# Kernel tuning notes

Hardware: AMD Instinct MI355X
Metric: run time of the kernel (lower is better)

The kernel has to match this reference:

```python
import jax, jax.numpy as jnp
import numpy as np

B, S, C, H = 64, 512, 256, 128
P = S  # predict_length defaults to seq_length


def _linear_init(k, fan_in, fan_out):
    bound = 1.0 / np.sqrt(fan_in)
    kw, kb = jax.random.split(k)
    w = jax.random.uniform(kw, (fan_in, fan_out), minval=-bound, maxval=bound, dtype=jnp.float32)
    b = jax.random.uniform(kb, (fan_out,), minval=-bound, maxval=bound, dtype=jnp.float32)
    return w, b


def setup_inputs() -> dict:
    key = jax.random.key(0)
    ks = jax.random.split(key, 10)
    x = jax.random.normal(ks[0], (B, S, C), dtype=jnp.float32)
    wq1, bq1 = _linear_init(ks[1], S, H)
    wk1, bk1 = _linear_init(ks[2], S, H)
    wq2, bq2 = _linear_init(ks[3], S // 2, H)
    wk2, bk2 = _linear_init(ks[4], S // 2, H)
    wq3, bq3 = _linear_init(ks[5], S // 4, H)
    wk3, bk3 = _linear_init(ks[6], S // 4, H)
    wv, bv = _linear_init(ks[7], S, S)
    wo, bo = _linear_init(ks[8], S, P)
    return dict(x=x, wq1=wq1, bq1=bq1, wk1=wk1, bk1=bk1,
                wq2=wq2, bq2=bq2, wk2=wk2, bk2=bk2,
                wq3=wq3, bq3=bq3, wk3=wk3, bk3=bk3,
                wv=wv, bv=bv, wo=wo, bo=bo)


def _channel_attn(xl, wq, bq, wk, bk):
    # xl: [b', C, L]; q,k: [b', C, H]; returns softmax channel-attention [b', C, C]
    q = xl @ wq + bq
    k = xl @ wk + bk
    scores = jnp.einsum('bch,bdh->bcd', q, k) / jnp.sqrt(jnp.asarray(H, q.dtype))
    return jax.nn.softmax(scores, axis=-1)


def reference(x, wq1, bq1, wk1, bk1, wq2, bq2, wk2, bk2, wq3, bq3, wk3, bk3, wv, bv, wo, bo):
    b, s, c = x.shape
    x1 = jnp.swapaxes(x, -2, -1)                                   # [B, C, S]
    x2 = jnp.swapaxes(x.reshape(b * 2, s // 2, c), -2, -1)          # [2B, C, S/2]
    x3 = jnp.swapaxes(x.reshape(b * 4, s // 4, c), -2, -1)          # [4B, C, S/4]
    a1 = _channel_attn(x1, wq1, bq1, wk1, bk1)                      # [B, C, C]
    a2 = _channel_attn(x2, wq2, bq2, wk2, bk2).reshape(b, 2, c, c).mean(axis=1)
    a3 = _channel_attn(x3, wq3, bq3, wk3, bk3).reshape(b, 4, c, c).mean(axis=1)
    stacked = jnp.stack([a1, a2, a3], axis=0)                       # [3, B, C, C]
    gate = jax.nn.softmax(stacked, axis=0)                          # softmax over scales
    attn = (stacked * gate).sum(axis=0)                             # gated multi-scale combine [B, C, C]
    v = x1 @ wv + bv                                                # [B, C, S]
    out = (attn @ v) @ wo + bo                                      # [B, C, P]
    return jnp.swapaxes(out, -2, -1)                                # [B, P, C]
```

## Files before the change

kernel.cpp:

```cpp
#include <hip/hip_runtime.h>
#include <hip/hip_bf16.h>


typedef __attribute__((ext_vector_type(8))) short bf16x8;
typedef __attribute__((ext_vector_type(4))) float f32x4;
typedef __attribute__((ext_vector_type(8))) unsigned short ushort8;

typedef __attribute__((address_space(1))) void* as1vp;
typedef __attribute__((address_space(3))) void* as3vp;

__device__ __forceinline__ void gl2lds16(const void* g, void* l) {
  __builtin_amdgcn_global_load_lds((as1vp)(void*)g, (as3vp)l, 16, 0, 0);
}

__device__ __forceinline__ float bf2f(unsigned short u) {
  union { unsigned int i; float f; } v; v.i = ((unsigned int)u) << 16; return v.f;
}
__device__ __forceinline__ unsigned short f2bf(float f) {
  union { float f; unsigned int i; } v; v.f = f;
  unsigned int r = v.i + 0x7FFFu + ((v.i >> 16) & 1u);
  return (unsigned short)(r >> 16);
}
__device__ __forceinline__ unsigned long long pack4bf(float a, float b, float c, float d) {
  return (unsigned long long)f2bf(a) | ((unsigned long long)f2bf(b) << 16) |
         ((unsigned long long)f2bf(c) << 32) | ((unsigned long long)f2bf(d) << 48);
}

__global__ void __launch_bounds__(256) tcast_all(
    const float* __restrict__ x,
    const float* __restrict__ wq1, const float* __restrict__ wk1,
    const float* __restrict__ wq2, const float* __restrict__ wk2,
    const float* __restrict__ wq3, const float* __restrict__ wk3,
    const float* __restrict__ wv, const float* __restrict__ wo,
    unsigned short* __restrict__ XT,
    unsigned short* __restrict__ W1, unsigned short* __restrict__ W2,
    unsigned short* __restrict__ W3, unsigned short* __restrict__ WVNT,
    unsigned short* __restrict__ WOT) {
  const int bid = blockIdx.x;
  const int t = threadIdx.x;
  if (bid >= 2168) {
    long i0 = (long)(bid - 2168) * 2048 + t * 8;
    f32x4 a = *(const f32x4*)(wv + i0);
    f32x4 b = *(const f32x4*)(wv + i0 + 4);
    ushort8 o;
#pragma unroll
    for (int j = 0; j < 4; ++j) { o[j] = f2bf(a[j]); o[4 + j] = f2bf(b[j]); }
    *(ushort8*)(WVNT + i0) = o;
    return;
  }
  __shared__ float lds[64][68];
  const float* S; unsigned short* D; int R, Cc, r0, c0, rowoff = 0;
  if (bid < 2048) {
    int bz = bid >> 5, i = bid & 31;
    S = x + (long)bz * 131072; D = XT + (long)bz * 131072;
    R = 512; Cc = 256; r0 = (i & 7) * 64; c0 = (i >> 3) * 64;
  } else {
    int wb = bid - 2048;
    if (wb < 32) {
      int m = wb >> 4, i = wb & 15;
      S = m ? wk1 : wq1; D = W1; R = 512; Cc = 128;
      r0 = (i & 7) * 64; c0 = (i >> 3) * 64; rowoff = m * 128;
    } else if (wb < 48) {
      int m = (wb - 32) >> 3, i = (wb - 32) & 7;
      S = m ? wk2 : wq2; D = W2; R = 256; Cc = 128;
      r0 = (i & 3) * 64; c0 = (i >> 2) * 64; rowoff = m * 128;
    } else if (wb < 56) {
      int m = (wb - 48) >> 2, i = (wb - 48) & 3;
      S = m ? wk3 : wq3; D = W3; R = 128; Cc = 128;
      r0 = (i & 1) * 64; c0 = (i >> 1) * 64; rowoff = m * 128;
    } else {
      int i = wb - 56; S = wo; D = WOT; R = 512; Cc = 512;
      r0 = (i & 7) * 64; c0 = (i >> 3) * 64;
    }
  }
  {
    const int row = t >> 2, cq = (t & 3) * 16;
    const float* Sp = S + (long)(r0 + row) * Cc + c0 + cq;
#pragma unroll
    for (int j = 0; j < 4; ++j)
      *(f32x4*)&lds[row][cq + j * 4] = *(const f32x4*)(Sp + j * 4);
  }
  __syncthreads();
  {
    const int rq = (t & 15) * 4, ccb = t >> 4;
#pragma unroll
    for (int j = 0; j < 4; ++j) {
      int cc = ccb + j * 16;
      *(unsigned long long*)(D + (long)(c0 + cc + rowoff) * R + r0 + rq) =
          pack4bf(lds[rq][cc], lds[rq + 1][cc], lds[rq + 2][cc], lds[rq + 3][cc]);
    }
  }
}

__global__ void __launch_bounds__(1024) projscore(
    const unsigned short* __restrict__ XT,
    const unsigned short* __restrict__ W1, const unsigned short* __restrict__ W2,
    const unsigned short* __restrict__ W3,
    const unsigned short* __restrict__ WOT, const unsigned short* __restrict__ WVNT,
    unsigned short* __restrict__ WVOT, float* __restrict__ BVO,
    const float* __restrict__ bv,
    unsigned short* __restrict__ A1F, unsigned short* __restrict__ A2F,
    unsigned short* __restrict__ A3F,
    const float* __restrict__ bq1, const float* __restrict__ bk1,
    const float* __restrict__ bq2, const float* __restrict__ bk2,
    const float* __restrict__ bq3, const float* __restrict__ bk3) {
  extern __shared__ char smem[];
  const int z = blockIdx.z;
  const int t = threadIdx.x, lane = t & 63, wid = t >> 6;

  if (z >= 464) {
    int p0 = (z - 464) * 128 + wid * 8;
    f32x4 b0 = *(const f32x4*)(bv + lane * 8);
    f32x4 b1 = *(const f32x4*)(bv + lane * 8 + 4);
#pragma unroll
    for (int i = 0; i < 8; ++i) {
      int p = p0 + i;
      bf16x8 wrow = *(const bf16x8*)(WOT + (long)p * 512 + lane * 8);
      float s = 0.0f;
#pragma unroll
      for (int j = 0; j < 4; ++j) {
        s += b0[j] * bf2f((unsigned short)wrow[j]);
        s += b1[j] * bf2f((unsigned short)wrow[4 + j]);
      }
#pragma unroll
      for (int off = 1; off < 64; off <<= 1) s += __shfl_xor(s, off, 64);
      if (lane == 0) BVO[p] = s;
    }
    return;
  }

  const int rS = t >> 3, sS = t & 7;

  if (z >= 448) {
    const int w = z - 448;
    const int m0 = (w >> 2) * 128, n0 = (w & 3) * 128;
    const unsigned short* Ab = WOT + (long)m0 * 512;
    const unsigned short* Bb = WVNT + (long)n0 * 512;
    const int wmb = (wid >> 2) * 32, wnb = (wid & 3) * 32;
    f32x4 acc[2][2] = {};
    for (int k0 = 0; k0 < 512; k0 += 64) {
      int sc = (sS ^ (rS & 7)) * 8;
      gl2lds16(Ab + (long)rS * 512 + k0 + sc, smem + t * 16);
      gl2lds16(Bb + (long)rS * 512 + k0 + sc, smem + 16384 + t * 16);
      __syncthreads();
#pragma unroll
      for (int kk = 0; kk < 2; ++kk) {
        const int slot = kk * 4 + (lane >> 4);
        bf16x8 af[2], bfr[2];
#pragma unroll
        for (int mi = 0; mi < 2; ++mi) {
          int row = wmb + mi * 16 + (lane & 15);
          af[mi] = *(const bf16x8*)(smem + row * 128 + 16 * (slot ^ (row & 7)));
        }
#pragma unroll
        for (int ni = 0; ni < 2; ++ni) {
          int row = wnb + ni * 16 + (lane & 15);
          bfr[ni] = *(const bf16x8*)(smem + 16384 + row * 128 + 16 * (slot ^ (row & 7)));
        }
#pragma unroll
        for (int mi = 0; mi < 2; ++mi)
#pragma unroll
          for (int ni = 0; ni < 2; ++ni)
            acc[mi][ni] = __builtin_amdgcn_mfma_f32_16x16x32_bf16(af[mi], bfr[ni], acc[mi][ni], 0, 0, 0);
      }
      __syncthreads();
    }
#pragma unroll
    for (int ni = 0; ni < 2; ++ni) {
      int col = n0 + wnb + ni * 16 + (lane & 15);
#pragma unroll
      for (int mi = 0; mi < 2; ++mi) {
        int rowb = m0 + wmb + mi * 16 + (lane >> 4) * 4;
#pragma unroll
        for (int r = 0; r < 4; ++r)
          WVOT[(long)(rowb + r) * 512 + col] = f2bf(acc[mi][ni][r]);
      }
    }
    return;
  }

  const unsigned short* Ab; const unsigned short* Bw; unsigned short* AF;
  const float *bq, *bk; int K; long sb;
  if (z < 64) {
    K = 512; Bw = W1; AF = A1F; sb = z; bq = bq1; bk = bk1;
    Ab = XT + (long)z * 131072;
  } else if (z < 192) {
    int u = z - 64; K = 256; Bw = W2; AF = A2F; sb = u; bq = bq2; bk = bk2;
    Ab = XT + (long)(u >> 1) * 131072 + (u & 1) * 256;
  } else {
    int u = z - 192; K = 128; Bw = W3; AF = A3F; sb = u; bq = bq3; bk = bk3;
    Ab = XT + (long)(u >> 2) * 131072 + (u & 3) * 128;
  }
  const int wmb = (wid >> 2) * 64, wnb = (wid & 3) * 64;

  auto stage = [&](int buf, int k0) {
    char* s = smem + buf * 65536;
#pragma unroll
    for (int i = 0; i < 2; ++i) {
      int row = i * 128 + rS;
      int sc = (sS ^ (row & 7)) * 8;
      gl2lds16(Ab + (long)row * 512 + k0 + sc, s + i * 16384 + t * 16);
      gl2lds16(Bw + (long)row * K + k0 + sc, s + 32768 + i * 16384 + t * 16);
    }
  };

  f32x4 acc[4][4] = {};
  const int nst = K >> 6;
  stage(0, 0);
  __syncthreads();
  int cur = 0;
  for (int j = 0; j < nst; ++j) {
    if (j + 1 < nst) stage(cur ^ 1, (j + 1) * 64);
    const char* s = smem + cur * 65536;
#pragma unroll
    for (int kk = 0; kk < 2; ++kk) {
      const int slot = kk * 4 + (lane >> 4);
      bf16x8 af[4], bfr[4];
#pragma unroll
      for (int mi = 0; mi < 4; ++mi) {
        int row = wmb + mi * 16 + (lane & 15);
        af[mi] = *(const bf16x8*)(s + row * 128 + 16 * (slot ^ (row & 7)));
      }
#pragma unroll
      for (int ni = 0; ni < 4; ++ni) {
        int row = wnb + ni * 16 + (lane & 15);
        bfr[ni] = *(const bf16x8*)(s + 32768 + row * 128 + 16 * (slot ^ (row & 7)));
      }
#pragma unroll
      for (int mi = 0; mi < 4; ++mi)
#pragma unroll
        for (int ni = 0; ni < 4; ++ni)
          acc[mi][ni] = __builtin_amdgcn_mfma_f32_16x16x32_bf16(bfr[ni], af[mi], acc[mi][ni], 0, 0, 0);
    }
    __syncthreads();
    cur ^= 1;
  }

  {
    const int chB = (wnb < 128) ? 0 : 65536;
    const float* bias = (wnb < 128) ? bq : bk;
    const int hbase = wnb & 127;
#pragma unroll
    for (int mi = 0; mi < 4; ++mi) {
      int rowm = wmb + mi * 16 + (lane & 15);
#pragma unroll
      for (int ni = 0; ni < 4; ++ni) {
        int h = hbase + ni * 16 + (lane >> 4) * 4;
        int addr = chB + (h >> 6) * 32768 + rowm * 128 +
                   16 * (((h & 63) >> 3) ^ (rowm & 7)) + (h & 7) * 2;
        *(unsigned long long*)(smem + addr) =
            pack4bf(acc[mi][ni][0] + bias[h], acc[mi][ni][1] + bias[h + 1],
                    acc[mi][ni][2] + bias[h + 2], acc[mi][ni][3] + bias[h + 3]);
      }
    }
  }
  __syncthreads();

  f32x4 acc2[16] = {};
  const int qrow = wid * 16 + (lane & 15);
#pragma unroll
  for (int kc = 0; kc < 2; ++kc)
#pragma unroll
    for (int kk = 0; kk < 2; ++kk) {
      const int slot = kk * 4 + (lane >> 4);
      bf16x8 qf = *(const bf16x8*)(smem + kc * 32768 + qrow * 128 + 16 * (slot ^ (qrow & 7)));
#pragma unroll
      for (int ni = 0; ni < 16; ++ni) {
        int krow = ni * 16 + (lane & 15);
        bf16x8 kf = *(const bf16x8*)(smem + 65536 + kc * 32768 + krow * 128 + 16 * (slot ^ (krow & 7)));
        acc2[ni] = __builtin_amdgcn_mfma_f32_16x16x32_bf16(qf, kf, acc2[ni], 0, 0, 0);
      }
    }

  const float sc = 0.088388347648318447f;
  {
    int m0idx = wid >> 2, quad = wid & 3;
    unsigned short* Of = AF + ((sb * 4 + m0idx) * 256 + quad * 64 + lane) * 64;
#pragma unroll
    for (int r = 0; r < 4; ++r) {
      float mx = -1e30f;
#pragma unroll
      for (int ni = 0; ni < 16; ++ni) mx = fmaxf(mx, acc2[ni][r]);
#pragma unroll
      for (int off = 1; off < 16; off <<= 1) mx = fmaxf(mx, __shfl_xor(mx, off, 64));
      float s = 0.0f;
#pragma unroll
      for (int ni = 0; ni < 16; ++ni) {
        float p = __expf((acc2[ni][r] - mx) * sc);
        acc2[ni][r] = p;
        s += p;
      }
#pragma unroll
      for (int off = 1; off < 16; off <<= 1) s += __shfl_xor(s, off, 64);
      float inv = 1.0f / s;
      ushort8 lo, hi;
#pragma unroll
      for (int j = 0; j < 8; ++j) {
        lo[j] = f2bf(acc2[j][r] * inv);
        hi[j] = f2bf(acc2[8 + j][r] * inv);
      }
      *(ushort8*)(Of + r * 16) = lo;
      *(ushort8*)(Of + r * 16 + 8) = hi;
    }
  }
}

__global__ void __launch_bounds__(256) gate_frag(
    const unsigned short* __restrict__ A1F, const unsigned short* __restrict__ A2F,
    const unsigned short* __restrict__ A3F, unsigned short* __restrict__ ATTN) {
  const long gid = (long)blockIdx.x * 256 + threadIdx.x;
  const long i = gid * 8;
  const int b = (int)(i >> 16);
  const int rest = (int)(i & 65535);
  ushort8 a1 = *(const ushort8*)(A1F + i);
  const long i2 = ((long)(2 * b) << 16) + rest;
  ushort8 a2a = *(const ushort8*)(A2F + i2);
  ushort8 a2b = *(const ushort8*)(A2F + i2 + 65536);
  const long i3 = ((long)(4 * b) << 16) + rest;
  ushort8 a3a = *(const ushort8*)(A3F + i3);
  ushort8 a3b = *(const ushort8*)(A3F + i3 + 65536);
  ushort8 a3c = *(const ushort8*)(A3F + i3 + 131072);
  ushort8 a3d = *(const ushort8*)(A3F + i3 + 196608);
  const int f = rest & 63;
  const int tl = (rest >> 6) & 255;
  const int m0idx = rest >> 14;
  const int quad = (tl >> 6) & 3;
  const int lane_s = tl & 63;
  const int r = f >> 4;
  const int u0 = f & 15;
  const int row = m0idx * 64 + quad * 16 + (lane_s >> 4) * 4 + r;
  unsigned short* Orow = ATTN + ((long)b << 16) + (long)row * 256 + (lane_s & 15);
#pragma unroll
  for (int j = 0; j < 8; ++j) {
    float A1 = bf2f(a1[j]);
    float A2 = 0.5f * (bf2f(a2a[j]) + bf2f(a2b[j]));
    float A3 = 0.25f * (bf2f(a3a[j]) + bf2f(a3b[j]) + bf2f(a3c[j]) + bf2f(a3d[j]));
    float m = fmaxf(A1, fmaxf(A2, A3));
    float e1 = __expf(A1 - m), e2 = __expf(A2 - m), e3 = __expf(A3 - m);
    Orow[(u0 + j) * 16] = f2bf((A1 * e1 + A2 * e2 + A3 * e3) / (e1 + e2 + e3));
  }
}

template <int F32OUT, int BIASMODE>
__global__ void __launch_bounds__(512) gemm8(
    const unsigned short* __restrict__ A, const unsigned short* __restrict__ B,
    void* __restrict__ OutV, const float* __restrict__ bias,
    int lda, int ldb, int K, long astr, long bstr, long ostr, int ldo) {
  extern __shared__ char smem[];
  const int t = threadIdx.x, lane = t & 63, wid = t >> 6;
  const int wmb = (wid >> 1) * 64, wnb = (wid & 1) * 64;
  const int m0 = blockIdx.y * 256, n0 = blockIdx.x * 128;
  const int bz = blockIdx.z;
  const unsigned short* Ab = A + (long)bz * astr + (long)m0 * lda;
  const unsigned short* Bb = B + (long)bz * bstr + (long)n0 * ldb;
  const int srow = t >> 3, ssl = t & 7;

  auto stage = [&](int buf, int k0) {
    char* s = smem + buf * 49152;
#pragma unroll
    for (int i = 0; i < 4; ++i) {
      int row = i * 64 + srow;
      gl2lds16(Ab + (long)row * lda + k0 + (ssl ^ (row & 7)) * 8, s + i * 8192 + t * 16);
    }
#pragma unroll
    for (int i = 0; i < 2; ++i) {
      int row = i * 64 + srow;
      gl2lds16(Bb + (long)row * ldb + k0 + (ssl ^ (row & 7)) * 8,
               s + 32768 + i * 8192 + t * 16);
    }
  };

  f32x4 acc[4][4] = {};
  const int nst = K >> 6;
  stage(0, 0);
  stage(1, 64);
  for (int j = 0; j < nst; ++j) {
    if (j + 1 < nst) asm volatile("s_waitcnt vmcnt(6)" ::: "memory");
    else             asm volatile("s_waitcnt vmcnt(0)" ::: "memory");
    __builtin_amdgcn_s_barrier();
    if (j + 2 < nst) stage((j + 2) % 3, (j + 2) * 64);
    const char* s = smem + (j % 3) * 49152;
#pragma unroll
    for (int kk = 0; kk < 2; ++kk) {
      const int slot = kk * 4 + (lane >> 4);
      bf16x8 af[4], bfr[4];
#pragma unroll
      for (int mi = 0; mi < 4; ++mi) {
        int row = wmb + mi * 16 + (lane & 15);
        af[mi] = *(const bf16x8*)(s + row * 128 + 16 * (slot ^ (row & 7)));
      }
#pragma unroll
      for (int ni = 0; ni < 4; ++ni) {
        int row = wnb + ni * 16 + (lane & 15);
        bfr[ni] = *(const bf16x8*)(s + 32768 + row * 128 + 16 * (slot ^ (row & 7)));
      }
#pragma unroll
      for (int mi = 0; mi < 4; ++mi)
#pragma unroll
        for (int ni = 0; ni < 4; ++ni)
          acc[mi][ni] = __builtin_amdgcn_mfma_f32_16x16x32_bf16(af[mi], bfr[ni], acc[mi][ni], 0, 0, 0);
    }
  }
#pragma unroll
  for (int mi = 0; mi < 4; ++mi) {
    int rowb = m0 + wmb + mi * 16 + (lane >> 4) * 4;
    float rb[4];
#pragma unroll
    for (int r = 0; r < 4; ++r) rb[r] = (BIASMODE == 2) ? bias[rowb + r] : 0.0f;
#pragma unroll
    for (int ni = 0; ni < 4; ++ni) {
      int col = n0 + wnb + ni * 16 + (lane & 15);
#pragma unroll
      for (int r = 0; r < 4; ++r) {
        float v = acc[mi][ni][r] + rb[r];
        if constexpr (F32OUT)
          ((float*)OutV)[(long)bz * ostr + (long)(rowb + r) * ldo + col] = v;
        else
          ((unsigned short*)OutV)[(long)bz * ostr + (long)(rowb + r) * ldo + col] = f2bf(v);
      }
    }
  }
}

extern "C" void kernel_launch(void* const* d_in, const int* in_sizes, int n_in,
                              void* d_out, int out_size, void* d_ws, size_t ws_size,
                              hipStream_t stream) {
  (void)in_sizes; (void)n_in; (void)out_size; (void)ws_size;
  const float* x   = (const float*)d_in[0];
  const float* wq1 = (const float*)d_in[1];
  const float* bq1 = (const float*)d_in[2];
  const float* wk1 = (const float*)d_in[3];
  const float* bk1 = (const float*)d_in[4];
  const float* wq2 = (const float*)d_in[5];
  const float* bq2 = (const float*)d_in[6];
  const float* wk2 = (const float*)d_in[7];
  const float* bk2 = (const float*)d_in[8];
  const float* wq3 = (const float*)d_in[9];
  const float* bq3 = (const float*)d_in[10];
  const float* wk3 = (const float*)d_in[11];
  const float* bk3 = (const float*)d_in[12];
  const float* wv  = (const float*)d_in[13];
  const float* bv  = (const float*)d_in[14];
  const float* wo  = (const float*)d_in[15];
  const float* bo  = (const float*)d_in[16];
  char* ws = (char*)d_ws;

  unsigned short* XT   = (unsigned short*)(ws + 0);
  unsigned short* WQK1 = (unsigned short*)(ws + 16777216);
  unsigned short* WQK2 = (unsigned short*)(ws + 17039360);
  unsigned short* WQK3 = (unsigned short*)(ws + 17170432);
  unsigned short* WOT  = (unsigned short*)(ws + 17235968);
  unsigned short* WVNT = (unsigned short*)(ws + 17760256);
  unsigned short* WVOT = (unsigned short*)(ws + 18284544);
  float*          BVO  = (float*)(ws + 18808832);
  unsigned short* A1F  = (unsigned short*)(ws + 18876416);
  unsigned short* A2F  = (unsigned short*)(ws + 27265024);
  unsigned short* A3F  = (unsigned short*)(ws + 44042240);
  unsigned short* ATTN = (unsigned short*)(ws + 77596672);
  unsigned short* XVT  = (unsigned short*)(ws + 18876416);

  tcast_all<<<dim3(2296), dim3(256), 0, stream>>>(
      x, wq1, wk1, wq2, wk2, wq3, wk3, wv, wo,
      XT, WQK1, WQK2, WQK3, WVNT, WOT);

  projscore<<<dim3(1, 1, 468), dim3(1024), 131072, stream>>>(
      XT, WQK1, WQK2, WQK3, WOT, WVNT, WVOT, BVO, bv,
      A1F, A2F, A3F, bq1, bk1, bq2, bk2, bq3, bk3);

  gate_frag<<<dim3(2048), dim3(256), 0, stream>>>(A1F, A2F, A3F, ATTN);

  gemm8<0, 2><<<dim3(2, 2, 64), dim3(512), 147456, stream>>>(
      WVOT, XT, XVT, BVO, 512, 512, 512, 0, 131072, 131072, 256);
  gemm8<1, 2><<<dim3(2, 2, 64), dim3(512), 147456, stream>>>(
      XVT, ATTN, d_out, bo, 256, 256, 256, 131072, 65536, 131072, 256);
}
```

Measured before the change: 95.30 us.

## Triple-buffer QK projection GEMM with 32-wide K tiles and fold softmax scale

The Q/K projection GEMM loop moves from a 64-wide K double buffer to a 32-wide K triple buffer. It uses explicit vmcnt waits and a single s_barrier per step, so loads stay two stages ahead of compute. This cuts LDS use per buffer and is meant to hide global-to-LDS latency better, at the cost of more iterations and barriers. The 1/sqrt(H) softmax scale is also folded into Q before the bf16 cast, which removes one multiply per score but changes where rounding happens.

```diff
diff --git a/kernel.cpp b/kernel.cpp
--- a/kernel.cpp
+++ b/kernel.cpp
@@ -25,6 +25,7 @@
   return (unsigned long long)f2bf(a) | ((unsigned long long)f2bf(b) << 16) |
          ((unsigned long long)f2bf(c) << 32) | ((unsigned long long)f2bf(d) << 48);
 }
+__device__ __forceinline__ int swz32(int row, int s) { return s ^ ((row >> 1) & 3); }
 
 __global__ void __launch_bounds__(256) tcast_all(
     const float* __restrict__ x,
@@ -129,7 +130,8 @@
     return;
   }
 
-  const int rS = t >> 3, sS = t & 7;
+  const int rS8 = t >> 3, sS8 = t & 7;
+  const int rS4 = t >> 2, sS4 = t & 3;
 
   if (z >= 448) {
     const int w = z - 448;
@@ -139,9 +141,9 @@
     const int wmb = (wid >> 2) * 32, wnb = (wid & 3) * 32;
     f32x4 acc[2][2] = {};
     for (int k0 = 0; k0 < 512; k0 += 64) {
-      int sc = (sS ^ (rS & 7)) * 8;
-      gl2lds16(Ab + (long)rS * 512 + k0 + sc, smem + t * 16);
-      gl2lds16(Bb + (long)rS * 512 + k0 + sc, smem + 16384 + t * 16);
+      int sc = (sS8 ^ (rS8 & 7)) * 8;
+      gl2lds16(Ab + (long)rS8 * 512 + k0 + sc, smem + t * 16);
+      gl2lds16(Bb + (long)rS8 * 512 + k0 + sc, smem + 16384 + t * 16);
       __syncthreads();
 #pragma unroll
       for (int kk = 0; kk < 2; ++kk) {
@@ -194,51 +196,47 @@
   const int wmb = (wid >> 2) * 64, wnb = (wid & 3) * 64;
 
   auto stage = [&](int buf, int k0) {
-    char* s = smem + buf * 65536;
-#pragma unroll
-    for (int i = 0; i < 2; ++i) {
-      int row = i * 128 + rS;
-      int sc = (sS ^ (row & 7)) * 8;
-      gl2lds16(Ab + (long)row * 512 + k0 + sc, s + i * 16384 + t * 16);
-      gl2lds16(Bw + (long)row * K + k0 + sc, s + 32768 + i * 16384 + t * 16);
-    }
+    char* s = smem + buf * 32768;
+    int sc = swz32(rS4, sS4) * 8;
+    gl2lds16(Ab + (long)rS4 * 512 + k0 + sc, s + t * 16);
+    gl2lds16(Bw + (long)rS4 * K + k0 + sc, s + 16384 + t * 16);
   };
 
   f32x4 acc[4][4] = {};
-  const int nst = K >> 6;
+  const int nst = K >> 5;
   stage(0, 0);
+  stage(1, 32);
+  for (int j = 0; j < nst; ++j) {
+    if (j + 1 < nst) asm volatile("s_waitcnt vmcnt(2)" ::: "memory");
+    else             asm volatile("s_waitcnt vmcnt(0)" ::: "memory");
+    __builtin_amdgcn_s_barrier();
+    if (j + 2 < nst) stage((j + 2) % 3, (j + 2) * 32);
+    const char* s = smem + (j % 3) * 32768;
+    const int kb = lane >> 4;
+    bf16x8 af[4], bfr[4];
+#pragma unroll
+    for (int mi = 0; mi < 4; ++mi) {
+      int row = wmb + mi * 16 + (lane & 15);
+      af[mi] = *(const bf16x8*)(s + row * 64 + (swz32(row, kb) << 4));
+    }
+#pragma unroll
+    for (int ni = 0; ni < 4; ++ni) {
+      int row = wnb + ni * 16 + (lane & 15);
+      bfr[ni] = *(const bf16x8*)(s + 16384 + row * 64 + (swz32(row, kb) << 4));
+    }
+#pragma unroll
+    for (int mi = 0; mi < 4; ++mi)
+#pragma unroll
+      for (int ni = 0; ni < 4; ++ni)
+        acc[mi][ni] = __builtin_amdgcn_mfma_f32_16x16x32_bf16(bfr[ni], af[mi], acc[mi][ni], 0, 0, 0);
+  }
   __syncthreads();
-  int cur = 0;
-  for (int j = 0; j < nst; ++j) {
-    if (j + 1 < nst) stage(cur ^ 1, (j + 1) * 64);
-    const char* s = smem + cur * 65536;
-#pragma unroll
-    for (int kk = 0; kk < 2; ++kk) {
-      const int slot = kk * 4 + (lane >> 4);
-      bf16x8 af[4], bfr[4];
-#pragma unroll
-      for (int mi = 0; mi < 4; ++mi) {
-        int row = wmb + mi * 16 + (lane & 15);
-        af[mi] = *(const bf16x8*)(s + row * 128 + 16 * (slot ^ (row & 7)));
-      }
-#pragma unroll
-      for (int ni = 0; ni < 4; ++ni) {
-        int row = wnb + ni * 16 + (lane & 15);
-        bfr[ni] = *(const bf16x8*)(s + 32768 + row * 128 + 16 * (slot ^ (row & 7)));
-      }
-#pragma unroll
-      for (int mi = 0; mi < 4; ++mi)
-#pragma unroll
-        for (int ni = 0; ni < 4; ++ni)
-          acc[mi][ni] = __builtin_amdgcn_mfma_f32_16x16x32_bf16(bfr[ni], af[mi], acc[mi][ni], 0, 0, 0);
-    }
-    __syncthreads();
-    cur ^= 1;
-  }
 
   {
-    const int chB = (wnb < 128) ? 0 : 65536;
-    const float* bias = (wnb < 128) ? bq : bk;
+    const bool isQ = (wnb < 128);
+    const float qsc = isQ ? 0.088388347648318447f : 1.0f;
+    const int chB = isQ ? 0 : 65536;
+    const float* bias = isQ ? bq : bk;
     const int hbase = wnb & 127;
 #pragma unroll
     for (int mi = 0; mi < 4; ++mi) {
@@ -249,8 +247,8 @@
         int addr = chB + (h >> 6) * 32768 + rowm * 128 +
                    16 * (((h & 63) >> 3) ^ (rowm & 7)) + (h & 7) * 2;
         *(unsigned long long*)(smem + addr) =
-            pack4bf(acc[mi][ni][0] + bias[h], acc[mi][ni][1] + bias[h + 1],
-                    acc[mi][ni][2] + bias[h + 2], acc[mi][ni][3] + bias[h + 3]);
+            pack4bf((acc[mi][ni][0] + bias[h]) * qsc, (acc[mi][ni][1] + bias[h + 1]) * qsc,
+                    (acc[mi][ni][2] + bias[h + 2]) * qsc, (acc[mi][ni][3] + bias[h + 3]) * qsc);
       }
     }
   }
@@ -272,7 +270,6 @@
       }
     }
 
-  const float sc = 0.088388347648318447f;
   {
     int m0idx = wid >> 2, quad = wid & 3;
     unsigned short* Of = AF + ((sb * 4 + m0idx) * 256 + quad * 64 + lane) * 64;
@@ -286,7 +283,7 @@
       float s = 0.0f;
 #pragma unroll
       for (int ni = 0; ni < 16; ++ni) {
-        float p = __expf((acc2[ni][r] - mx) * sc);
+        float p = __expf(acc2[ni][r] - mx);
         acc2[ni][r] = p;
         s += p;
       }
```

New measurement: 96.30 us. No clear change (+1.0%).
